# Kernel tuning notes

Hardware: AMD Instinct MI355X
Metric: run time of the kernel (lower is better)

Reference implementation:

```python
import jax, jax.numpy as jnp
import numpy as np

B, CIN, F, H, W = 4, 256, 128, 64, 64
EPS = 1e-5

def _conv1x1(x, Wm, b):
    # x: [B,C,H,W], Wm: [O,C] (1x1 conv kernel), b: [O]
    return jnp.einsum('bchw,oc->bohw', x, Wm) + b[None, :, None, None]

def setup_inputs() -> dict:
    key = jax.random.key(0)
    ks = jax.random.split(key, 11)
    s_in = 1.0 / np.sqrt(CIN)
    s_f = 1.0 / np.sqrt(F)
    return {
        'x':    jax.random.normal(ks[0], (B, CIN, H, W), jnp.float32),
        'Wg':   jax.random.normal(ks[1], (F, CIN), jnp.float32) * s_in,
        'bg':   jax.random.normal(ks[2], (F,), jnp.float32) * s_in,
        'Wt':   jax.random.normal(ks[3], (F, CIN), jnp.float32) * s_in,
        'bt':   jax.random.normal(ks[4], (F,), jnp.float32) * s_in,
        'Wp':   jax.random.normal(ks[5], (F, CIN), jnp.float32) * s_in,
        'bp':   jax.random.normal(ks[6], (F,), jnp.float32) * s_in,
        'Wz':   jax.random.normal(ks[7], (CIN, F), jnp.float32) * s_f,
        'bz':   jax.random.normal(ks[8], (CIN,), jnp.float32) * s_f,
        'ln_w': jax.random.normal(ks[9], (CIN, H, W), jnp.float32) * 0.1,
        'ln_b': jax.random.normal(ks[10], (CIN, H, W), jnp.float32) * 0.1,
    }

def reference(x, Wg, bg, Wt, bt, Wp, bp, Wz, bz, ln_w, ln_b):
    b, _, h, w = x.shape
    n = h * w
    # 1x1 conv projections
    g = _conv1x1(x, Wg, bg).reshape(b, F, n).transpose(0, 2, 1)      # [B,N,F]
    theta = _conv1x1(x, Wt, bt).reshape(b, F, n).transpose(0, 2, 1)  # [B,N,F]
    phi = _conv1x1(x, Wp, bp).reshape(b, F, n)                        # [B,F,N]
    # embedded-Gaussian affinity + softmax attention
    f = jnp.einsum('bnf,bfm->bnm', theta, phi)                        # [B,N,N]
    attn = jax.nn.softmax(f, axis=-1)
    y = jnp.einsum('bnm,bmf->bnf', attn, g)                           # [B,N,F]
    y = y.transpose(0, 2, 1).reshape(b, F, h, w)                      # [B,F,H,W]
    # output projection
    z = _conv1x1(y, Wz, bz)                                           # [B,CIN,H,W]
    # LayerNorm over (C,H,W) per sample, affine params shaped [C,H,W]
    mu = jnp.mean(z, axis=(1, 2, 3), keepdims=True)
    var = jnp.var(z, axis=(1, 2, 3), keepdims=True)
    z = (z - mu) * jax.lax.rsqrt(var + EPS)
    z = z * ln_w[None] + ln_b[None]
    return z + x
```

## Files before the change

### kernel.cpp

```cpp
#include <hip/hip_runtime.h>
#include <hip/hip_bf16.h>
#include <stdint.h>

#define CIN 256
#define FDIM 128
#define NSP 4096
#define EPS 1e-5f

typedef __attribute__((ext_vector_type(8))) short short8;
typedef __attribute__((ext_vector_type(4))) float f32x4;
typedef __attribute__((ext_vector_type(16))) float f32x16;

__device__ __forceinline__ short f2bf(float f) {
  union { float f; uint32_t u; } v; v.f = f;
  uint32_t r = v.u + 0x7fffu + ((v.u >> 16) & 1u);
  return (short)(r >> 16);
}
__device__ __forceinline__ float bf2f(short h) {
  union { uint32_t u; float f; } v; v.u = ((uint32_t)(uint16_t)h) << 16;
  return v.f;
}
__device__ __forceinline__ uint32_t pk2bf(float a, float b) {
  union { __hip_bfloat162 h; uint32_t u; } cv;
  cv.h = __float22bfloat162_rn(float2{a, b});
  return cv.u;
}

__global__ void prep_weights(const float* __restrict__ Wg, const float* __restrict__ Wt,
                             const float* __restrict__ Wp, const float* __restrict__ Wz,
                             short* __restrict__ Wbf, short* __restrict__ Wzbf) {
  int idx = blockIdx.x * 256 + threadIdx.x;
  if (idx < 384 * 256) {
    int row = idx >> 8, col = idx & 255;
    float v;
    if (row < 128)       v = Wt[row * 256 + col];
    else if (row < 256)  v = Wp[(row - 128) * 256 + col];
    else                 v = Wg[(row - 256) * 256 + col];
    Wbf[idx] = f2bf(v);
  } else {
    int j = idx - 384 * 256;
    if (j < 256 * 128) Wzbf[j] = f2bf(Wz[j]);
  }
}

__global__ void prep_xT(const float* __restrict__ x, short* __restrict__ xT) {
  __shared__ float tile[32][33];
  int b = blockIdx.z, c0 = blockIdx.y * 32, n0 = blockIdx.x * 32;
  int r = threadIdx.x >> 5, c = threadIdx.x & 31;
  const float* xb = x + (size_t)b * CIN * NSP;
#pragma unroll
  for (int k = 0; k < 4; k++)
    tile[r + 8 * k][c] = xb[(size_t)(c0 + r + 8 * k) * NSP + n0 + c];
  __syncthreads();
  short* xTb = xT + (size_t)b * NSP * CIN;
#pragma unroll
  for (int k = 0; k < 4; k++)
    xTb[(size_t)(n0 + r + 8 * k) * CIN + c0 + c] = f2bf(tile[c][r + 8 * k]);
}

__global__ void __launch_bounds__(256)
proj_kernel(const short* __restrict__ xT, const short* __restrict__ Wbf,
            const float* __restrict__ bt, const float* __restrict__ bp,
            const float* __restrict__ bg,
            short* __restrict__ theta, short* __restrict__ Kb, short* __restrict__ gT) {
  __shared__ short lds[5120];
  int bx = blockIdx.x;
  int b = bx >> 7;
  int n0 = (bx & 127) << 5;
  int p = blockIdx.y;
  int t = threadIdx.x, w = t >> 6, lane = t & 63, l15 = lane & 15, quad = lane >> 4;

  const short* arow = xT + (size_t)(b * NSP + n0 + (w & 1) * 16 + l15) * CIN;
  short8 a[8];
#pragma unroll
  for (int s = 0; s < 8; s++) a[s] = *(const short8*)(arow + s * 32 + quad * 8);

  const short* Wsrc = Wbf + p * 128 * 256;
  f32x4 zero = {0.f, 0.f, 0.f, 0.f};
  f32x4 acc[4];
#pragma unroll
  for (int i = 0; i < 4; i++) acc[i] = zero;

#pragma unroll
  for (int s = 0; s < 8; s++) {
#pragma unroll
    for (int ft = 0; ft < 4; ft++) {
      int ftg = (w >> 1) * 4 + ft;
      short8 bfr = *(const short8*)(Wsrc + (ftg * 16 + l15) * 256 + s * 32 + quad * 8);
      acc[ft] = __builtin_amdgcn_mfma_f32_16x16x32_bf16(a[s], bfr, acc[ft], 0, 0, 0);
    }
  }

  const float* bias = (p == 0) ? bt : (p == 1) ? bp : bg;
  if (p < 2) {
#pragma unroll
    for (int ft = 0; ft < 4; ft++) {
      int ftg = (w >> 1) * 4 + ft;
      float bv = bias[ftg * 16 + l15];
#pragma unroll
      for (int rr = 0; rr < 4; rr++) {
        int n = (w & 1) * 16 + quad * 4 + rr;
        lds[n * 136 + ftg * 16 + l15] = f2bf(acc[ft][rr] + bv);
      }
    }
    __syncthreads();
    short* dst = ((p == 0) ? theta : Kb) + (size_t)(b * NSP + n0) * FDIM;
#pragma unroll
    for (int i = 0; i < 2; i++) {
      int flat = t + 256 * i;
      int row = flat >> 4, ch = flat & 15;
      *(short8*)(dst + (size_t)row * FDIM + ch * 8) = *(const short8*)(lds + row * 136 + ch * 8);
    }
  } else {
#pragma unroll
    for (int ft = 0; ft < 4; ft++) {
      int ftg = (w >> 1) * 4 + ft;
      float bv = bias[ftg * 16 + l15];
#pragma unroll
      for (int rr = 0; rr < 4; rr++) {
        int n = (w & 1) * 16 + quad * 4 + rr;
        lds[(ftg * 16 + l15) * 40 + n] = f2bf(acc[ft][rr] + bv);
      }
    }
    __syncthreads();
    short* dst = gT + (size_t)b * FDIM * NSP + n0;
#pragma unroll
    for (int i = 0; i < 2; i++) {
      int flat = t + 256 * i;
      int f = flat >> 2, c = flat & 3;
      *(short8*)(dst + (size_t)f * NSP + c * 8) = *(const short8*)(lds + f * 40 + c * 8);
    }
  }
}

__global__ void __launch_bounds__(256, 2)
flash_kernel(const short* __restrict__ thetab, const short* __restrict__ Kb,
             const short* __restrict__ gT, short* __restrict__ opart,
             float* __restrict__ lpart) {
  __shared__ __attribute__((aligned(16))) char smem[75776];
  short* Klds = (short*)smem;
  short* Vlds = (short*)(smem + 34816);
  float* Om   = (float*)smem;
  float* lsm  = (float*)(smem + 65536);

  const int bx = blockIdx.x;
  const int b  = bx >> 7;
  const int r  = bx & 127;
  const int q0 = (r >> 2) << 7;
  const int kc = r & 3;
  const int t = threadIdx.x, w = t >> 6, lane = t & 63;
  const int l31 = lane & 31, h = lane >> 5;
  const int qw = q0 + (w & 1) * 64;
  const int ck = w >> 1;

  const short* Qsrc = thetab + (size_t)b * NSP * FDIM;
  const short* Ksrc = Kb + (size_t)b * NSP * FDIM;
  const short* Vsrc = gT + (size_t)b * FDIM * NSP;

  short8 qf0[8], qf1[8];
#pragma unroll
  for (int s = 0; s < 8; s++) {
    qf0[s] = *(const short8*)(Qsrc + (size_t)(qw + l31) * FDIM + s * 16 + h * 8);
    qf1[s] = *(const short8*)(Qsrc + (size_t)(qw + 32 + l31) * FDIM + s * 16 + h * 8);
  }

  f32x16 O0[4], O1[4];
#pragma unroll
  for (int i = 0; i < 4; i++) {
#pragma unroll
    for (int j = 0; j < 16; j++) { O0[i][j] = 0.f; O1[i][j] = 0.f; }
  }
  float lsum0 = 0.f, lsum1 = 0.f;

  const int kA0 = kc << 10;

  {
    const int kA = kA0, kB = kA0 + 512;
#pragma unroll
    for (int rep = 0; rep < 2; rep++) {
      int flat = t + 256 * rep;
      int row = flat >> 4, c = flat & 15;
      *(short8*)(Klds + row * 136 + c * 8) =
          *(const short8*)(Ksrc + (size_t)(kA + row) * FDIM + c * 8);
      *(short8*)(Klds + 4352 + row * 136 + c * 8) =
          *(const short8*)(Ksrc + (size_t)(kB + row) * FDIM + c * 8);
      int f = flat >> 2, c2 = flat & 3;
      *(short8*)(Vlds + f * 40 + c2 * 8) =
          *(const short8*)(Vsrc + (size_t)f * NSP + kA + c2 * 8);
      *(short8*)(Vlds + 5120 + f * 40 + c2 * 8) =
          *(const short8*)(Vsrc + (size_t)f * NSP + kB + c2 * 8);
    }
  }
  __syncthreads();

  for (int it = 0; it < 16; ++it) {
    const int cur = it & 1;
    const short* Kl = Klds + (cur * 2 + ck) * 4352;
    const short* Vl = Vlds + (cur * 2 + ck) * 5120;

    f32x16 S0, S1;
#pragma unroll
    for (int j = 0; j < 16; j++) { S0[j] = 0.f; S1[j] = 0.f; }
#pragma unroll
    for (int s = 0; s < 8; s++) {
      short8 ak = *(const short8*)(Kl + l31 * 136 + s * 16 + h * 8);
      S0 = __builtin_amdgcn_mfma_f32_32x32x16_bf16(ak, qf0[s], S0, 0, 0, 0);
      S1 = __builtin_amdgcn_mfma_f32_32x32x16_bf16(ak, qf1[s], S1, 0, 0, 0);
    }

    short8 Af0[2], Af1[2];
#pragma unroll
    for (int qb = 0; qb < 2; qb++) {
      float p[16];
      float ls = 0.f;
#pragma unroll
      for (int i = 0; i < 16; i++) {
        p[i] = __expf(qb ? S1[i] : S0[i]);
        ls += p[i];
      }
      if (qb) lsum1 += ls; else lsum0 += ls;
      short8* Af = qb ? Af1 : Af0;
#pragma unroll
      for (int tt = 0; tt < 2; tt++) {
        const int rb = tt * 8;
        uint32_t pk01 = pk2bf(p[rb + 0], p[rb + 1]);
        uint32_t pk23 = pk2bf(p[rb + 2], p[rb + 3]);
        uint32_t pk45 = pk2bf(p[rb + 4], p[rb + 5]);
        uint32_t pk67 = pk2bf(p[rb + 6], p[rb + 7]);
        uint32_t r0 = (uint32_t)__shfl_xor((int)(h ? pk01 : pk45), 32, 64);
        uint32_t r1 = (uint32_t)__shfl_xor((int)(h ? pk23 : pk67), 32, 64);
        union { uint32_t u[4]; short8 v; } u;
        u.u[0] = h ? r0 : pk01;
        u.u[1] = h ? r1 : pk23;
        u.u[2] = h ? pk45 : r0;
        u.u[3] = h ? pk67 : r1;
        Af[tt] = u.v;
      }
    }

    const bool more = (it + 1 < 16);
    short8 nk0[2], nk1[2], nv0[2], nv1[2];
    if (more) {
      const int kA = kA0 + (it + 1) * 32, kB = kA + 512;
#pragma unroll
      for (int rep = 0; rep < 2; rep++) {
        int flat = t + 256 * rep;
        int row = flat >> 4, c = flat & 15;
        nk0[rep] = *(const short8*)(Ksrc + (size_t)(kA + row) * FDIM + c * 8);
        nk1[rep] = *(const short8*)(Ksrc + (size_t)(kB + row) * FDIM + c * 8);
        int f = flat >> 2, c2 = flat & 3;
        nv0[rep] = *(const short8*)(Vsrc + (size_t)f * NSP + kA + c2 * 8);
        nv1[rep] = *(const short8*)(Vsrc + (size_t)f * NSP + kB + c2 * 8);
      }
    }

#pragma unroll
    for (int ft = 0; ft < 4; ft++) {
#pragma unroll
      for (int tt = 0; tt < 2; tt++) {
        short8 bv = *(const short8*)(Vl + (ft * 32 + l31) * 40 + tt * 16 + h * 8);
        O0[ft] = __builtin_amdgcn_mfma_f32_32x32x16_bf16(Af0[tt], bv, O0[ft], 0, 0, 0);
        O1[ft] = __builtin_amdgcn_mfma_f32_32x32x16_bf16(Af1[tt], bv, O1[ft], 0, 0, 0);
      }
    }

    if (more) {
      short* Kd = Klds + ((it + 1) & 1) * 2 * 4352;
      short* Vd = Vlds + ((it + 1) & 1) * 2 * 5120;
#pragma unroll
      for (int rep = 0; rep < 2; rep++) {
        int flat = t + 256 * rep;
        int row = flat >> 4, c = flat & 15;
        *(short8*)(Kd + row * 136 + c * 8) = nk0[rep];
        *(short8*)(Kd + 4352 + row * 136 + c * 8) = nk1[rep];
        int f = flat >> 2, c2 = flat & 3;
        *(short8*)(Vd + f * 40 + c2 * 8) = nv0[rep];
        *(short8*)(Vd + 5120 + f * 40 + c2 * 8) = nv1[rep];
      }
      __syncthreads();
    }
  }

  lsum0 += __shfl_xor(lsum0, 32, 64);
  lsum1 += __shfl_xor(lsum1, 32, 64);

  __syncthreads();
  if (w >= 2) {
    float* dst = Om + (size_t)(w - 2) * 8192;
#pragma unroll
    for (int qb = 0; qb < 2; qb++) {
#pragma unroll
      for (int ft = 0; ft < 4; ft++) {
#pragma unroll
        for (int reg = 0; reg < 16; reg++) {
          int rowq = qb * 32 + (reg & 3) + 8 * (reg >> 2) + 4 * h;
          dst[rowq * 128 + ft * 32 + l31] = qb ? O1[ft][reg] : O0[ft][reg];
        }
      }
    }
    if (h == 0) {
      lsm[(w - 2) * 64 + l31] = lsum0;
      lsm[(w - 2) * 64 + 32 + l31] = lsum1;
    }
  }
  __syncthreads();
  if (w < 2) {
    const float* src = Om + (size_t)w * 8192;
    short* od = opart + ((size_t)(kc * 4 + b) * NSP + qw) * FDIM;
#pragma unroll
    for (int qb = 0; qb < 2; qb++) {
#pragma unroll
      for (int ft = 0; ft < 4; ft++) {
#pragma unroll
        for (int reg = 0; reg < 16; reg++) {
          int rowq = qb * 32 + (reg & 3) + 8 * (reg >> 2) + 4 * h;
          float v = (qb ? O1[ft][reg] : O0[ft][reg]) + src[rowq * 128 + ft * 32 + l31];
          od[(size_t)rowq * FDIM + ft * 32 + l31] = f2bf(v);
        }
      }
    }
    if (h == 0) {
      size_t lb = (size_t)(kc * 4 + b) * NSP + qw;
      lpart[lb + l31] = lsum0 + lsm[w * 64 + l31];
      lpart[lb + 32 + l31] = lsum1 + lsm[w * 64 + 32 + l31];
    }
  }
}

__global__ void __launch_bounds__(256)
zproj_kernel(const short* __restrict__ opart, const float* __restrict__ lpart,
             const short* __restrict__ Wzbf, const float* __restrict__ bz,
             short* __restrict__ zb, float* __restrict__ psums) {
  __shared__ short ldsT[128 * 40];
  __shared__ float wsum[4][2];
  int bx = blockIdx.x;
  int b = bx >> 7;
  int n0 = (bx & 127) << 5;
  int ch0 = blockIdx.y * 128;
  int t = threadIdx.x, w = t >> 6, lane = t & 63, l15 = lane & 15, quad = lane >> 4;

  int row = n0 + (w & 1) * 16 + l15;
  float L = 0.f;
#pragma unroll
  for (int kcc = 0; kcc < 4; kcc++) L += lpart[(size_t)(kcc * 4 + b) * NSP + row];
  float inv = 1.0f / L;

  short8 a[4];
#pragma unroll
  for (int s = 0; s < 4; s++) {
    float accv[8] = {0, 0, 0, 0, 0, 0, 0, 0};
#pragma unroll
    for (int kcc = 0; kcc < 4; kcc++) {
      short8 v = *(const short8*)(opart + ((size_t)(kcc * 4 + b) * NSP + row) * FDIM + s * 32 + quad * 8);
#pragma unroll
      for (int j = 0; j < 8; j++) accv[j] += bf2f(v[j]);
    }
    short8 av;
#pragma unroll
    for (int j = 0; j < 8; j++) av[j] = f2bf(accv[j] * inv);
    a[s] = av;
  }

  f32x4 zero = {0.f, 0.f, 0.f, 0.f};
  f32x4 acc[4];
#pragma unroll
  for (int i = 0; i < 4; i++) acc[i] = zero;
#pragma unroll
  for (int s = 0; s < 4; s++) {
#pragma unroll
    for (int ct = 0; ct < 4; ct++) {
      int co = ch0 + (w >> 1) * 64 + ct * 16 + l15;
      short8 bfr = *(const short8*)(Wzbf + (size_t)co * FDIM + s * 32 + quad * 8);
      acc[ct] = __builtin_amdgcn_mfma_f32_16x16x32_bf16(a[s], bfr, acc[ct], 0, 0, 0);
    }
  }

  float s1 = 0.0f, s2 = 0.0f;
#pragma unroll
  for (int ct = 0; ct < 4; ct++) {
    int cg = (w >> 1) * 64 + ct * 16 + l15;
    float bv = bz[ch0 + cg];
#pragma unroll
    for (int rr = 0; rr < 4; rr++) {
      float v = acc[ct][rr] + bv;
      s1 += v; s2 += v * v;
      ldsT[cg * 40 + (w & 1) * 16 + quad * 4 + rr] = f2bf(v);
    }
  }
#pragma unroll
  for (int off = 32; off >= 1; off >>= 1) {
    s1 += __shfl_xor(s1, off, 64);
    s2 += __shfl_xor(s2, off, 64);
  }
  if (lane == 0) { wsum[w][0] = s1; wsum[w][1] = s2; }
  __syncthreads();
  if (t == 0) {
    int bid = blockIdx.y * 512 + bx;
    psums[bid * 2] = wsum[0][0] + wsum[1][0] + wsum[2][0] + wsum[3][0];
    psums[bid * 2 + 1] = wsum[0][1] + wsum[1][1] + wsum[2][1] + wsum[3][1];
  }
  short* dst = zb + (size_t)b * CIN * NSP + (size_t)ch0 * NSP + n0;
#pragma unroll
  for (int i = 0; i < 2; i++) {
    int flat = t + 256 * i;
    int c = flat >> 2, ch = flat & 3;
    *(short8*)(dst + (size_t)c * NSP + ch * 8) = *(const short8*)(ldsT + c * 40 + ch * 8);
  }
}

__global__ void reduce_sums(const float* __restrict__ psums, float* __restrict__ sums) {
  __shared__ float red[8];
  int t = threadIdx.x;
  if (t < 8) red[t] = 0.f;
  __syncthreads();
  for (int i = t; i < 1024; i += 256) {
    int b = (i & 511) >> 7;
    atomicAdd(&red[b * 2], psums[i * 2]);
    atomicAdd(&red[b * 2 + 1], psums[i * 2 + 1]);
  }
  __syncthreads();
  if (t < 8) sums[t] = red[t];
}

__global__ void __launch_bounds__(256)
finalize_kernel(const short* __restrict__ zbuf, const float* __restrict__ x,
                const float* __restrict__ lnw, const float* __restrict__ lnb,
                const float* __restrict__ sums, float* __restrict__ out) {
  int gid = blockIdx.x * 256 + threadIdx.x;
  size_t e0 = (size_t)gid * 8;
  int b = (int)(e0 >> 20);
  size_t ib = e0 & ((size_t)(1u << 20) - 1);
  float mean = sums[b * 2] * (1.0f / 1048576.0f);
  float var = sums[b * 2 + 1] * (1.0f / 1048576.0f) - mean * mean;
  float rs = rsqrtf(var + EPS);
  short8 zv = *(const short8*)(zbuf + e0);
#pragma unroll
  for (int k = 0; k < 8; k++) {
    float z = bf2f(zv[k]);
    out[e0 + k] = (z - mean) * rs * lnw[ib + k] + lnb[ib + k] + x[e0 + k];
  }
}

extern "C" void kernel_launch(void* const* d_in, const int* in_sizes, int n_in,
                              void* d_out, int out_size, void* d_ws, size_t ws_size,
                              hipStream_t stream) {
  const float* x   = (const float*)d_in[0];
  const float* Wg  = (const float*)d_in[1];
  const float* bg  = (const float*)d_in[2];
  const float* Wt  = (const float*)d_in[3];
  const float* bt  = (const float*)d_in[4];
  const float* Wp  = (const float*)d_in[5];
  const float* bp  = (const float*)d_in[6];
  const float* Wz  = (const float*)d_in[7];
  const float* bz  = (const float*)d_in[8];
  const float* lnw = (const float*)d_in[9];
  const float* lnb = (const float*)d_in[10];
  float* out = (float*)d_out;

  char* ws = (char*)d_ws;
  short* Wbf    = (short*)(ws);
  short* Wzbf   = (short*)(ws + 196608);
  short* xT     = (short*)(ws + 262144);
  short* opart  = (short*)(ws + 262144);
  float* lpart  = (float*)(ws + 17039360);
  short* thetab = (short*)(ws + 17301504);
  short* Kb     = (short*)(ws + 21495808);
  short* gT     = (short*)(ws + 25690112);
  short* zb     = (short*)(ws + 17301504);
  float* sums   = (float*)(ws + 29884416);
  float* psums  = (float*)(ws + 29884448);

  prep_weights<<<512, 256, 0, stream>>>(Wg, Wt, Wp, Wz, Wbf, Wzbf);
  prep_xT<<<dim3(128, 8, 4), 256, 0, stream>>>(x, xT);
  proj_kernel<<<dim3(512, 3), 256, 0, stream>>>(xT, Wbf, bt, bp, bg, thetab, Kb, gT);
  flash_kernel<<<512, 256, 0, stream>>>(thetab, Kb, gT, opart, lpart);
  zproj_kernel<<<dim3(512, 2), 256, 0, stream>>>(opart, lpart, Wzbf, bz, zb, psums);
  reduce_sums<<<1, 256, 0, stream>>>(psums, sums);
  finalize_kernel<<<2048, 256, 0, stream>>>(zb, x, lnw, lnb, sums, out);
}
```

Measured before the change: 210.4 us.

## Stage K/V via direct global-to-LDS loads with XOR swizzle, fold log2e into theta

K and V tiles now go straight from global memory into LDS with global_load_lds, replacing the register round-trip. Padded layouts become XOR-swizzled ones to avoid bank conflicts, which shrinks LDS use. The prefetch for the next tile is issued at the top of each iteration. log2(e) is folded into the theta weights and bias so the softmax can use exp2 directly. The risk is that the async LDS writes are only covered by the end-of-iteration barrier, and the swizzle indexing must exactly match the MFMA read pattern.

```diff
diff --git a/kernel.cpp b/kernel.cpp
--- a/kernel.cpp
+++ b/kernel.cpp
@@ -6,6 +6,7 @@
 #define FDIM 128
 #define NSP 4096
 #define EPS 1e-5f
+#define LOG2E 1.4426950408889634f
 
 typedef __attribute__((ext_vector_type(8))) short short8;
 typedef __attribute__((ext_vector_type(4))) float f32x4;
@@ -24,6 +25,11 @@
   union { __hip_bfloat162 h; uint32_t u; } cv;
   cv.h = __float22bfloat162_rn(float2{a, b});
   return cv.u;
+}
+__device__ __forceinline__ void gload16(const void* g, void* l) {
+  __builtin_amdgcn_global_load_lds(
+      (const __attribute__((address_space(1))) unsigned int*)g,
+      (__attribute__((address_space(3))) unsigned int*)l, 16, 0, 0);
 }
 
 __global__ void prep_weights(const float* __restrict__ Wg, const float* __restrict__ Wt,
@@ -33,7 +39,7 @@
   if (idx < 384 * 256) {
     int row = idx >> 8, col = idx & 255;
     float v;
-    if (row < 128)       v = Wt[row * 256 + col];
+    if (row < 128)       v = Wt[row * 256 + col] * LOG2E;
     else if (row < 256)  v = Wp[(row - 128) * 256 + col];
     else                 v = Wg[(row - 256) * 256 + col];
     Wbf[idx] = f2bf(v);
@@ -97,6 +103,7 @@
     for (int ft = 0; ft < 4; ft++) {
       int ftg = (w >> 1) * 4 + ft;
       float bv = bias[ftg * 16 + l15];
+      if (p == 0) bv *= LOG2E;
 #pragma unroll
       for (int rr = 0; rr < 4; rr++) {
         int n = (w & 1) * 16 + quad * 4 + rr;
@@ -137,9 +144,9 @@
 flash_kernel(const short* __restrict__ thetab, const short* __restrict__ Kb,
              const short* __restrict__ gT, short* __restrict__ opart,
              float* __restrict__ lpart) {
-  __shared__ __attribute__((aligned(16))) char smem[75776];
+  __shared__ __attribute__((aligned(16))) char smem[66048];
   short* Klds = (short*)smem;
-  short* Vlds = (short*)(smem + 34816);
+  short* Vlds = (short*)(smem + 32768);
   float* Om   = (float*)smem;
   float* lsm  = (float*)(smem + 65536);
 
@@ -174,36 +181,42 @@
 
   const int kA0 = kc << 10;
 
-  {
-    const int kA = kA0, kB = kA0 + 512;
-#pragma unroll
-    for (int rep = 0; rep < 2; rep++) {
-      int flat = t + 256 * rep;
-      int row = flat >> 4, c = flat & 15;
-      *(short8*)(Klds + row * 136 + c * 8) =
-          *(const short8*)(Ksrc + (size_t)(kA + row) * FDIM + c * 8);
-      *(short8*)(Klds + 4352 + row * 136 + c * 8) =
-          *(const short8*)(Ksrc + (size_t)(kB + row) * FDIM + c * 8);
-      int f = flat >> 2, c2 = flat & 3;
-      *(short8*)(Vlds + f * 40 + c2 * 8) =
-          *(const short8*)(Vsrc + (size_t)f * NSP + kA + c2 * 8);
-      *(short8*)(Vlds + 5120 + f * 40 + c2 * 8) =
-          *(const short8*)(Vsrc + (size_t)f * NSP + kB + c2 * 8);
-    }
-  }
+  auto stage = [&](int kA, int buf) {
+#pragma unroll
+    for (int e = 0; e < 4; e++) {
+      int kr = (w << 2) + e;
+      int row = (kr << 2) + (lane >> 4);
+      int key = kA + (row & 31) + ((row >> 5) << 9);
+      int gcol = (lane & 15) ^ (row & 15);
+      gload16(Ksrc + (size_t)key * FDIM + gcol * 8,
+              Klds + buf * 8192 + kr * 512);
+    }
+#pragma unroll
+    for (int e = 0; e < 4; e++) {
+      int vr = (w << 2) + e;
+      int f = (vr << 3) + (lane >> 3);
+      int m = (lane & 7) ^ (f & 7);
+      int key = kA + ((m >> 2) << 9) + ((m & 3) << 3);
+      gload16(Vsrc + (size_t)f * NSP + key,
+              Vlds + buf * 8192 + vr * 512);
+    }
+  };
+
+  stage(kA0, 0);
   __syncthreads();
 
   for (int it = 0; it < 16; ++it) {
+    if (it + 1 < 16) stage(kA0 + (it + 1) * 32, (it + 1) & 1);
     const int cur = it & 1;
-    const short* Kl = Klds + (cur * 2 + ck) * 4352;
-    const short* Vl = Vlds + (cur * 2 + ck) * 5120;
+    const short* Kl = Klds + cur * 8192 + ck * 4096;
+    const short* Vl = Vlds + cur * 8192;
 
     f32x16 S0, S1;
 #pragma unroll
     for (int j = 0; j < 16; j++) { S0[j] = 0.f; S1[j] = 0.f; }
 #pragma unroll
     for (int s = 0; s < 8; s++) {
-      short8 ak = *(const short8*)(Kl + l31 * 136 + s * 16 + h * 8);
+      short8 ak = *(const short8*)(Kl + l31 * 128 + ((((s << 1) | h) ^ (l31 & 15)) << 3));
       S0 = __builtin_amdgcn_mfma_f32_32x32x16_bf16(ak, qf0[s], S0, 0, 0, 0);
       S1 = __builtin_amdgcn_mfma_f32_32x32x16_bf16(ak, qf1[s], S1, 0, 0, 0);
     }
@@ -215,7 +228,7 @@
       float ls = 0.f;
 #pragma unroll
       for (int i = 0; i < 16; i++) {
-        p[i] = __expf(qb ? S1[i] : S0[i]);
+        p[i] = exp2f(qb ? S1[i] : S0[i]);
         ls += p[i];
       }
       if (qb) lsum1 += ls; else lsum0 += ls;
@@ -238,47 +251,18 @@
       }
     }
 
-    const bool more = (it + 1 < 16);
-    short8 nk0[2], nk1[2], nv0[2], nv1[2];
-    if (more) {
-      const int kA = kA0 + (it + 1) * 32, kB = kA + 512;
-#pragma unroll
-      for (int rep = 0; rep < 2; rep++) {
-        int flat = t + 256 * rep;
-        int row = flat >> 4, c = flat & 15;
-        nk0[rep] = *(const short8*)(Ksrc + (size_t)(kA + row) * FDIM + c * 8);
-        nk1[rep] = *(const short8*)(Ksrc + (size_t)(kB + row) * FDIM + c * 8);
-        int f = flat >> 2, c2 = flat & 3;
-        nv0[rep] = *(const short8*)(Vsrc + (size_t)f * NSP + kA + c2 * 8);
-        nv1[rep] = *(const short8*)(Vsrc + (size_t)f * NSP + kB + c2 * 8);
-      }
-    }
-
 #pragma unroll
     for (int ft = 0; ft < 4; ft++) {
 #pragma unroll
       for (int tt = 0; tt < 2; tt++) {
-        short8 bv = *(const short8*)(Vl + (ft * 32 + l31) * 40 + tt * 16 + h * 8);
+        short8 bv = *(const short8*)(Vl + ((ft * 32 + l31) << 6) +
+                                     ((((ck << 2) | (tt << 1) | h) ^ (l31 & 7)) << 3));
         O0[ft] = __builtin_amdgcn_mfma_f32_32x32x16_bf16(Af0[tt], bv, O0[ft], 0, 0, 0);
         O1[ft] = __builtin_amdgcn_mfma_f32_32x32x16_bf16(Af1[tt], bv, O1[ft], 0, 0, 0);
       }
     }
 
-    if (more) {
-      short* Kd = Klds + ((it + 1) & 1) * 2 * 4352;
-      short* Vd = Vlds + ((it + 1) & 1) * 2 * 5120;
-#pragma unroll
-      for (int rep = 0; rep < 2; rep++) {
-        int flat = t + 256 * rep;
-        int row = flat >> 4, c = flat & 15;
-        *(short8*)(Kd + row * 136 + c * 8) = nk0[rep];
-        *(short8*)(Kd + 4352 + row * 136 + c * 8) = nk1[rep];
-        int f = flat >> 2, c2 = flat & 3;
-        *(short8*)(Vd + f * 40 + c2 * 8) = nv0[rep];
-        *(short8*)(Vd + 5120 + f * 40 + c2 * 8) = nv1[rep];
-      }
-      __syncthreads();
-    }
+    __syncthreads();
   }
 
   lsum0 += __shfl_xor(lsum0, 32, 64);
```

After: 211.7 us. About the same (+0.6%).
